# Kernel tuning notes

Measured on AMD Instinct MI355X. Metric: run time of the kernel, lower is better.

The kernel has to match this reference:

```python
import jax, jax.numpy as jnp
import numpy as np

N, C_IN, H, W = 16, 32, 512, 512
C_OUT, K, STRIDE = 32, 3, 1


def setup_inputs() -> dict:
    key = jax.random.key(0)
    k1, k2, k3 = jax.random.split(key, 3)
    x = jax.random.normal(k1, (N, C_IN, H, W), dtype=jnp.float32)
    weight = jax.random.normal(k2, (C_OUT, C_IN, K, K), dtype=jnp.float32) * 0.05
    bias = jax.random.normal(k3, (C_OUT,), dtype=jnp.float32) * 0.05
    return {"x": x, "weight": weight, "bias": bias}


def reference(x, weight, bias):
    # Direct 2D convolution, NCHW / OIHW, stride 1, no padding (VALID),
    # matching the module's per-pixel multiply+sum with padding=0.
    out = jax.lax.conv_general_dilated(
        x, weight,
        window_strides=(STRIDE, STRIDE),
        padding="VALID",
        dimension_numbers=("NCHW", "OIHW", "NCHW"),
    )
    return out + bias[None, :, None, None]
```

## Files before the change

kernel.cpp:

```cpp
#include <hip/hip_runtime.h>


namespace {
constexpr int NI    = 16;
constexpr int C_IN  = 32;
constexpr int HI    = 512;
constexpr int WI    = 512;
constexpr int C_OUT = 32;
constexpr int HO    = 510;
constexpr int WO    = 510;

constexpr int RT    = 6;
constexpr int PT    = 256;
constexpr int XCOLS = 264;
constexpr int PSTR  = 40;
constexpr int SLOTS = 3;
constexpr int SLOTW = XCOLS * PSTR;
constexpr int HIWI  = HI * WI;
constexpr int NT    = 1024;
}

typedef __attribute__((ext_vector_type(4))) float  floatx4;
typedef __attribute__((ext_vector_type(8))) __bf16 bf16x8;
typedef __attribute__((ext_vector_type(8))) unsigned short ushortx8;

__global__ void conv_wprep(const float* __restrict__ w, __bf16* __restrict__ ws) {
  const int t = threadIdx.x;
  for (int i = t; i < 9 * 2 * 64 * 8; i += 256) {
    const int j    = i & 7;
    const int lane = (i >> 3) & 63;
    const int h    = (i >> 9) & 1;
    const int tap  = i >> 10;
    const int co   = h * 16 + (lane & 15);
    const int ci   = (lane >> 4) * 8 + j;
    ws[i] = (__bf16)w[(co * C_IN + ci) * 9 + tap];
  }
}

__global__ __launch_bounds__(NT, 4)
void conv3x3_mfma(const float* __restrict__ x, const __bf16* __restrict__ ws,
                  const float* __restrict__ bias, float* __restrict__ out) {
  __shared__ __bf16 lds[SLOTS * SLOTW];

  const int t    = threadIdx.x;
  const int lane = t & 63;
  const int wv   = t >> 6;
  const int quad = lane >> 4;
  const int l16  = lane & 15;
  const int ch   = wv >> 3;
  const int w8   = wv & 7;

  const int x0 = blockIdx.x * PT;
  const int y0 = blockIdx.y * RT;
  const int n  = blockIdx.z;

  const float* xn = x + (size_t)n * C_IN * HIWI;

  const int ps   = t & 255;
  const int cq   = t >> 8;
  const int gofs = (cq * 8) * HIWI + x0 + ps;
  const int lofs = ps * PSTR + cq * 8;

  const bool hw  = (wv < 4);
  const int hci  = t >> 3;
  const int hpx  = 256 + (t & 7);
  int hgx = x0 + hpx; if (hgx > WI - 1) hgx = WI - 1;
  const int hgo  = hci * HIWI + hgx;
  const int hlo  = hpx * PSTR + hci;

  auto issue = [&](int gr, float (&b)[8], float& h) {
    const float* rb = xn + (size_t)(y0 + gr) * WI;
#pragma unroll
    for (int k = 0; k < 8; ++k) b[k] = rb[gofs + k * HIWI];
    if (hw) h = rb[hgo];
  };
  auto commit = [&](int slot, float (&b)[8], float h) {
    __bf16* s = lds + slot * SLOTW;
    union { __bf16 bb[8]; ushortx8 u; } pk;
#pragma unroll
    for (int k = 0; k < 8; ++k) pk.bb[k] = (__bf16)b[k];
    *reinterpret_cast<ushortx8*>(s + lofs) = pk.u;
    if (hw) s[hlo] = (__bf16)h;
  };

  {
    float p0[8], p1[8], p2[8];
    float h0 = 0.f, h1 = 0.f, h2 = 0.f;
    issue(0, p0, h0); issue(1, p1, h1); issue(2, p2, h2);
    commit(0, p0, h0); commit(1, p1, h1); commit(2, p2, h2);
  }

  bf16x8 afrag[9];
#pragma unroll
  for (int tap = 0; tap < 9; ++tap)
    afrag[tap] = *reinterpret_cast<const bf16x8*>(ws + ((tap * 2 + ch) * 64 + lane) * 8);

  float bv[4];
#pragma unroll
  for (int r = 0; r < 4; ++r)
    bv[r] = bias[ch * 16 + quad * 4 + r];

  __syncthreads();

  const int pxb = x0 + w8 * 32 + l16;
  floatx4 acc[3][2];
  float buf[8]; float hb = 0.f;

#pragma unroll
  for (int ir = 0; ir < RT + 2; ++ir) {
    if (ir + 3 < RT + 2) issue(ir + 3, buf, hb);

    if (ir < RT) {
#pragma unroll
      for (int f = 0; f < 2; ++f)
        acc[ir % 3][f] = floatx4{bv[0], bv[1], bv[2], bv[3]};
    }

    bf16x8 bf[2][3];
    const __bf16* sl = lds + (ir % SLOTS) * SLOTW + (w8 * 32 + l16) * PSTR + quad * 8;
#pragma unroll
    for (int f = 0; f < 2; ++f)
#pragma unroll
      for (int kx = 0; kx < 3; ++kx)
        bf[f][kx] = *reinterpret_cast<const bf16x8*>(sl + (f * 16 + kx) * PSTR);

#pragma unroll
    for (int ky = 0; ky < 3; ++ky) {
      const int o = ir - ky;
      if (o < 0 || o >= RT) continue;
#pragma unroll
      for (int kx = 0; kx < 3; ++kx)
#pragma unroll
        for (int f = 0; f < 2; ++f)
          acc[o % 3][f] = __builtin_amdgcn_mfma_f32_16x16x32_bf16(
              afrag[ky * 3 + kx], bf[f][kx], acc[o % 3][f], 0, 0, 0);
    }

    if (ir >= 2) {
      const int o = ir - 2;
      float* op = out + ((size_t)(n * C_OUT + ch * 16 + quad * 4) * HO + (y0 + o)) * WO + pxb;
#pragma unroll
      for (int f = 0; f < 2; ++f) {
        if (pxb + f * 16 < WO) {
#pragma unroll
          for (int r = 0; r < 4; ++r)
            op[r * (HO * WO) + f * 16] = acc[o % 3][f][r];
        }
      }
    }

    __syncthreads();
    if (ir + 3 < RT + 2)
      commit(ir % SLOTS, buf, hb);
  }
}

extern "C" void kernel_launch(void* const* d_in, const int* in_sizes, int n_in,
                              void* d_out, int out_size, void* d_ws, size_t ws_size,
                              hipStream_t stream) {
  const float* x    = (const float*)d_in[0];
  const float* w    = (const float*)d_in[1];
  const float* bias = (const float*)d_in[2];
  float* out        = (float*)d_out;
  __bf16* ws        = (__bf16*)d_ws;

  conv_wprep<<<dim3(1), 256, 0, stream>>>(w, ws);

  dim3 grid(WI / PT, HO / RT, NI);
  conv3x3_mfma<<<grid, NT, 0, stream>>>(x, ws, bias, out);
}
```

Baseline: 905.0 us.

## Widen conv tile to full image row and drop halo column loads

Each block now covers the full 512-pixel input row instead of a 256-pixel half plus an 8-column halo. Each thread loads 16 channels per row, and each wave computes four 16-pixel fragments instead of two. This removes the duplicated halo loads and the separate halo path, and halves the number of blocks. In exchange the LDS tile grows beyond 64 KB and now needs dynamic shared memory with a raised attribute. Fewer blocks fit per CU, and the larger accumulator set adds register pressure, both of which can cut latency hiding.

Result: slower. 976.9 us (+7.9%).

```diff
diff --git a/kernel.cpp b/kernel.cpp
--- a/kernel.cpp
+++ b/kernel.cpp
@@ -11,11 +11,12 @@
 constexpr int WO    = 510;
 
 constexpr int RT    = 6;
-constexpr int PT    = 256;
-constexpr int XCOLS = 264;
+constexpr int PT    = 512;
+constexpr int XCOLS = 514;
 constexpr int PSTR  = 40;
 constexpr int SLOTS = 3;
 constexpr int SLOTW = XCOLS * PSTR;
+constexpr int LDS_BYTES = SLOTS * SLOTW * 2;
 constexpr int HIWI  = HI * WI;
 constexpr int NT    = 1024;
 }
@@ -40,7 +41,7 @@
 __global__ __launch_bounds__(NT, 4)
 void conv3x3_mfma(const float* __restrict__ x, const __bf16* __restrict__ ws,
                   const float* __restrict__ bias, float* __restrict__ out) {
-  __shared__ __bf16 lds[SLOTS * SLOTW];
+  extern __shared__ __bf16 lds[];
 
   const int t    = threadIdx.x;
   const int lane = t & 63;
@@ -50,44 +51,34 @@
   const int ch   = wv >> 3;
   const int w8   = wv & 7;
 
-  const int x0 = blockIdx.x * PT;
-  const int y0 = blockIdx.y * RT;
-  const int n  = blockIdx.z;
+  const int y0 = blockIdx.x * RT;
+  const int n  = blockIdx.y;
 
   const float* xn = x + (size_t)n * C_IN * HIWI;
 
-  const int ps   = t & 255;
-  const int cq   = t >> 8;
-  const int gofs = (cq * 8) * HIWI + x0 + ps;
-  const int lofs = ps * PSTR + cq * 8;
+  const int ps   = t & 511;
+  const int cq   = t >> 9;
+  const int gofs = (cq * 16) * HIWI + ps;
+  const int lofs = ps * PSTR + cq * 16;
 
-  const bool hw  = (wv < 4);
-  const int hci  = t >> 3;
-  const int hpx  = 256 + (t & 7);
-  int hgx = x0 + hpx; if (hgx > WI - 1) hgx = WI - 1;
-  const int hgo  = hci * HIWI + hgx;
-  const int hlo  = hpx * PSTR + hci;
-
-  auto issue = [&](int gr, float (&b)[8], float& h) {
+  auto issue = [&](int gr, float (&b)[16]) {
     const float* rb = xn + (size_t)(y0 + gr) * WI;
 #pragma unroll
-    for (int k = 0; k < 8; ++k) b[k] = rb[gofs + k * HIWI];
-    if (hw) h = rb[hgo];
+    for (int k = 0; k < 16; ++k) b[k] = rb[gofs + k * HIWI];
   };
-  auto commit = [&](int slot, float (&b)[8], float h) {
-    __bf16* s = lds + slot * SLOTW;
-    union { __bf16 bb[8]; ushortx8 u; } pk;
+  auto commit = [&](int slot, float (&b)[16]) {
+    __bf16* s = lds + slot * SLOTW + lofs;
+    union { __bf16 bb[16]; ushortx8 u[2]; } pk;
 #pragma unroll
-    for (int k = 0; k < 8; ++k) pk.bb[k] = (__bf16)b[k];
-    *reinterpret_cast<ushortx8*>(s + lofs) = pk.u;
-    if (hw) s[hlo] = (__bf16)h;
+    for (int k = 0; k < 16; ++k) pk.bb[k] = (__bf16)b[k];
+    *reinterpret_cast<ushortx8*>(s)     = pk.u[0];
+    *reinterpret_cast<ushortx8*>(s + 8) = pk.u[1];
   };
 
   {
-    float p0[8], p1[8], p2[8];
-    float h0 = 0.f, h1 = 0.f, h2 = 0.f;
-    issue(0, p0, h0); issue(1, p1, h1); issue(2, p2, h2);
-    commit(0, p0, h0); commit(1, p1, h1); commit(2, p2, h2);
+    float p0[16], p1[16], p2[16];
+    issue(0, p0); issue(1, p1); issue(2, p2);
+    commit(0, p0); commit(1, p1); commit(2, p2);
   }
 
   bf16x8 afrag[9];
@@ -102,45 +93,43 @@
 
   __syncthreads();
 
-  const int pxb = x0 + w8 * 32 + l16;
-  floatx4 acc[3][2];
-  float buf[8]; float hb = 0.f;
+  const int pxb = w8 * 64 + l16;
+  floatx4 acc[3][4];
+  float buf[16];
 
 #pragma unroll
   for (int ir = 0; ir < RT + 2; ++ir) {
-    if (ir + 3 < RT + 2) issue(ir + 3, buf, hb);
+    if (ir + 3 <= RT + 1) issue(ir + 3, buf);
 
     if (ir < RT) {
 #pragma unroll
-      for (int f = 0; f < 2; ++f)
+      for (int f = 0; f < 4; ++f)
         acc[ir % 3][f] = floatx4{bv[0], bv[1], bv[2], bv[3]};
     }
 
-    bf16x8 bf[2][3];
-    const __bf16* sl = lds + (ir % SLOTS) * SLOTW + (w8 * 32 + l16) * PSTR + quad * 8;
+    const __bf16* sl = lds + (ir % SLOTS) * SLOTW + (w8 * 64 + l16) * PSTR + quad * 8;
 #pragma unroll
-    for (int f = 0; f < 2; ++f)
+    for (int kx = 0; kx < 3; ++kx) {
+      bf16x8 bfr[4];
 #pragma unroll
-      for (int kx = 0; kx < 3; ++kx)
-        bf[f][kx] = *reinterpret_cast<const bf16x8*>(sl + (f * 16 + kx) * PSTR);
-
+      for (int f = 0; f < 4; ++f)
+        bfr[f] = *reinterpret_cast<const bf16x8*>(sl + (f * 16 + kx) * PSTR);
 #pragma unroll
-    for (int ky = 0; ky < 3; ++ky) {
-      const int o = ir - ky;
-      if (o < 0 || o >= RT) continue;
+      for (int ky = 0; ky < 3; ++ky) {
+        const int o = ir - ky;
+        if (o < 0 || o >= RT) continue;
 #pragma unroll
-      for (int kx = 0; kx < 3; ++kx)
-#pragma unroll
-        for (int f = 0; f < 2; ++f)
+        for (int f = 0; f < 4; ++f)
           acc[o % 3][f] = __builtin_amdgcn_mfma_f32_16x16x32_bf16(
-              afrag[ky * 3 + kx], bf[f][kx], acc[o % 3][f], 0, 0, 0);
+              afrag[ky * 3 + kx], bfr[f], acc[o % 3][f], 0, 0, 0);
+      }
     }
 
     if (ir >= 2) {
       const int o = ir - 2;
       float* op = out + ((size_t)(n * C_OUT + ch * 16 + quad * 4) * HO + (y0 + o)) * WO + pxb;
 #pragma unroll
-      for (int f = 0; f < 2; ++f) {
+      for (int f = 0; f < 4; ++f) {
         if (pxb + f * 16 < WO) {
 #pragma unroll
           for (int r = 0; r < 4; ++r)
@@ -150,8 +139,8 @@
     }
 
     __syncthreads();
-    if (ir + 3 < RT + 2)
-      commit(ir % SLOTS, buf, hb);
+    if (ir + 3 <= RT + 1)
+      commit(ir % SLOTS, buf);
   }
 }
 
@@ -164,8 +153,15 @@
   float* out        = (float*)d_out;
   __bf16* ws        = (__bf16*)d_ws;
 
+  static bool lds_cfg = false;
+  if (!lds_cfg) {
+    hipFuncSetAttribute((const void*)conv3x3_mfma,
+                        hipFuncAttributeMaxDynamicSharedMemorySize, LDS_BYTES);
+    lds_cfg = true;
+  }
+
   conv_wprep<<<dim3(1), 256, 0, stream>>>(w, ws);
 
-  dim3 grid(WI / PT, HO / RT, NI);
-  conv3x3_mfma<<<grid, NT, 0, stream>>>(x, ws, bias, out);
+  dim3 grid(HO / RT, NI);
+  conv3x3_mfma<<<grid, NT, LDS_BYTES, stream>>>(x, ws, bias, out);
 }
```
